# Optimization experiments

Hardware: AMD Instinct MI355X
Metric: run time of the kernel (lower is better)

## Reference

```python
import jax, jax.numpy as jnp
import numpy as np

D_MODEL = 512
N_HEADS = 8
HEAD_DIM = D_MODEL // N_HEADS
SIGMA = 0.05
LOW_RANK = 8


def setup_inputs() -> dict:
    key = jax.random.key(0)
    ks = jax.random.split(key, 16)
    B, N, Q, K = 4, 8, 256, 1024
    s = 0.02
    return {
        "query": jax.random.normal(ks[0], (B, N, Q, D_MODEL), jnp.float32),
        "key_value": jax.random.normal(ks[1], (B, N, K, D_MODEL), jnp.float32),
        "query_pos": jax.random.uniform(ks[2], (B, Q, 3), jnp.float32),
        "key_pos": jax.random.uniform(ks[3], (B, K, 3), jnp.float32),
        "key_mask": jnp.ones((B, K), dtype=bool),
        "Wq": jax.random.normal(ks[4], (D_MODEL, D_MODEL), jnp.float32) * s,
        "bq": jnp.zeros((D_MODEL,), jnp.float32),
        "Wk": jax.random.normal(ks[5], (D_MODEL, D_MODEL), jnp.float32) * s,
        "bk": jnp.zeros((D_MODEL,), jnp.float32),
        "Wv": jax.random.normal(ks[6], (D_MODEL, D_MODEL), jnp.float32) * s,
        "bv": jnp.zeros((D_MODEL,), jnp.float32),
        "Wo": jax.random.normal(ks[7], (D_MODEL, D_MODEL), jnp.float32) * s,
        "bo": jnp.zeros((D_MODEL,), jnp.float32),
        "Wqb": jax.random.normal(ks[8], (3, LOW_RANK), jnp.float32) * 0.5,
        "Wkb": jax.random.normal(ks[9], (3, LOW_RANK), jnp.float32) * 0.5,
    }


def reference(query, key_value, query_pos, key_pos, key_mask,
              Wq, bq, Wk, bk, Wv, bv, Wo, bo, Wqb, Wkb):
    B, N, Qn, _ = query.shape
    Kn = key_value.shape[2]
    scale = HEAD_DIM ** -0.5

    # projections -> [B, N, L, H, Dh]
    q = (query @ Wq + bq).reshape(B, N, Qn, N_HEADS, HEAD_DIM)
    k = (key_value @ Wk + bk).reshape(B, N, Kn, N_HEADS, HEAD_DIM)
    v = (key_value @ Wv + bv).reshape(B, N, Kn, N_HEADS, HEAD_DIM)

    logits = jnp.einsum('bnqhd,bnkhd->bnhqk', q, k) * scale

    # Gaussian distance bias: [B, Q, K]
    dist2 = jnp.sum((query_pos[:, :, None, :] - key_pos[:, None, :, :]) ** 2, axis=-1)
    sigma2 = max(SIGMA * SIGMA, 1e-6)
    dist_bias = -dist2 / (2.0 * sigma2)

    # low-rank leadfield bias: [B, Q, K]
    qb = query_pos @ Wqb  # [B, Q, R]
    kb = key_pos @ Wkb    # [B, K, R]
    lf_bias = jnp.einsum('bqr,bkr->bqk', qb, kb) / max(float(LOW_RANK) ** 0.5, 1.0)

    logits = logits + (dist_bias + lf_bias)[:, None, None, :, :]
    logits = jnp.where(key_mask[:, None, None, None, :], logits, -10000.0)

    attn = jax.nn.softmax(logits, axis=-1)
    out = jnp.einsum('bnhqk,bnkhd->bnqhd', attn, v).reshape(B, N, Qn, D_MODEL)
    return out @ Wo + bo
```

## Files before the change

kernel.cpp:

```cpp
#include <hip/hip_runtime.h>
#include <hip/hip_bf16.h>
#include <stdint.h>


typedef __attribute__((ext_vector_type(8))) short bf16x8;
typedef __attribute__((ext_vector_type(4))) float f32x4;
typedef __attribute__((ext_vector_type(2))) float f32x2;

__device__ __forceinline__ unsigned short f2b(float f){
    unsigned int u = __builtin_bit_cast(unsigned int, f);
    unsigned int r = u + 0x7fffu + ((u >> 16) & 1u);
    return (unsigned short)(r >> 16);
}
__device__ __forceinline__ float b2f(unsigned short h){
    unsigned int u = ((unsigned int)h) << 16;
    return __builtin_bit_cast(float, u);
}

__device__ __forceinline__ unsigned cvtpk2(float lo, float hi){
    unsigned r;
    asm("v_cvt_pk_bf16_f32 %0, %1, %2" : "=v"(r) : "v"(lo), "v"(hi));
    return r;
}

__device__ __forceinline__ int swz(int row, int byteInRow){
    return row*128 + (byteInRow ^ ((row & 7) << 4));
}

#define GLDS16(g, l) __builtin_amdgcn_global_load_lds( \
    (const __attribute__((address_space(1))) void*)(g), \
    (__attribute__((address_space(3))) void*)(l), 16, 0, 0)

template<int CTRL>
__device__ __forceinline__ float dpp_mov(float x){
    return __builtin_bit_cast(float,
        __builtin_amdgcn_update_dpp(0, __builtin_bit_cast(int, x), CTRL, 0xF, 0xF, true));
}
__device__ __forceinline__ float grp16_sum(float x){
    x += dpp_mov<0xB1>(x);
    x += dpp_mov<0x4E>(x);
    x += dpp_mov<0x141>(x);
    x += dpp_mov<0x140>(x);
    return x;
}

__global__ __launch_bounds__(256) void wt4_kernel(
    const float* __restrict__ Wq, const float* __restrict__ Wk,
    const float* __restrict__ Wv, const float* __restrict__ Wo,
    unsigned short* __restrict__ WtBase){
    __shared__ float tile[64][65];
    int kt = blockIdx.x, nt = blockIdx.y, wsel = blockIdx.z;
    const float* W = (wsel == 0) ? Wq : (wsel == 1) ? Wk : (wsel == 2) ? Wv : Wo;
    unsigned short* Wt = WtBase + (size_t)wsel * 262144;
    int tid = threadIdx.x;
    #pragma unroll
    for(int it=0; it<16; ++it){
        int idx = it*256 + tid;
        int r = idx >> 6, c = idx & 63;
        tile[r][c] = W[(kt*64 + r)*512 + nt*64 + c];
    }
    __syncthreads();
    #pragma unroll
    for(int it=0; it<16; ++it){
        int idx = it*256 + tid;
        int r = idx >> 6, c = idx & 63;
        Wt[(nt*64 + r)*512 + kt*64 + c] = f2b(tile[c][r]);
    }
}

__global__ __launch_bounds__(256) void posfeat2_kernel(
    const float* __restrict__ qpos, const float* __restrict__ kpos,
    const float* __restrict__ Wqb,  const float* __restrict__ Wkb,
    const int* __restrict__ mask,
    unsigned short* __restrict__ qaug,
    unsigned short* __restrict__ kaug){
    const float L2E = 1.4426950408889634f;
    const float S8  = 0.35355339059327373f;
    int id = blockIdx.x*256 + threadIdx.x;
    unsigned short o[32];
    #pragma unroll
    for(int i=0;i<32;++i) o[i] = 0;
    if(id < 1024){
        const float* p = qpos + id*3;
        float x = p[0], y = p[1], z = p[2];
        float qw[3] = {400.f*x, 400.f*y, 400.f*z};
        #pragma unroll
        for(int r=0;r<8;++r){
            float qb = x*Wqb[r] + y*Wqb[8+r] + z*Wqb[16+r];
            float c  = S8*qb;
            qw[0] += c*Wkb[r];
            qw[1] += c*Wkb[8+r];
            qw[2] += c*Wkb[16+r];
        }
        #pragma unroll
        for(int i=0;i<3;++i){
            float w = qw[i]*L2E;
            unsigned short h = f2b(w);
            unsigned short lo = f2b(w - b2f(h));
            o[i*3+0] = h; o[i*3+1] = h; o[i*3+2] = lo;
        }
        o[9] = f2b(1.0f); o[10] = f2b(1.0f);
        float cq = -200.0f*(x*x + y*y + z*z)*L2E;
        unsigned short ch = f2b(cq);
        o[11] = ch; o[12] = f2b(cq - b2f(ch));
        uint4* d = reinterpret_cast<uint4*>(qaug + (size_t)id*32);
        const uint4* s = reinterpret_cast<const uint4*>(o);
        d[0]=s[0]; d[1]=s[1]; d[2]=s[2]; d[3]=s[3];
    } else if(id < 5120){
        int k = id - 1024;
        const float* p = kpos + k*3;
        float c3[3] = {p[0], p[1], p[2]};
        float n2 = -200.0f*(c3[0]*c3[0] + c3[1]*c3[1] + c3[2]*c3[2])*L2E;
        if(!mask[k]) n2 = -50000.0f;
        #pragma unroll
        for(int i=0;i<3;++i){
            unsigned short h = f2b(c3[i]);
            unsigned short lo = f2b(c3[i] - b2f(h));
            o[i*3+0] = h; o[i*3+1] = lo; o[i*3+2] = h;
        }
        unsigned short nh = f2b(n2);
        o[9] = nh; o[10] = f2b(n2 - b2f(nh));
        o[11] = f2b(1.0f); o[12] = f2b(1.0f);
        uint4* d = reinterpret_cast<uint4*>(kaug + (size_t)k*32);
        const uint4* s = reinterpret_cast<const uint4*>(o);
        d[0]=s[0]; d[1]=s[1]; d[2]=s[2]; d[3]=s[3];
    }
}

__global__ __launch_bounds__(256) void cvt_kernel(
    const float* __restrict__ in, unsigned short* __restrict__ out, int n8){
    for(int id = blockIdx.x*256 + threadIdx.x; id < n8; id += gridDim.x*256){
        const float4* ip = reinterpret_cast<const float4*>(in) + (size_t)id*2;
        float4 a = ip[0], b = ip[1];
        uint4 w;
        w.x = cvtpk2(a.x, a.y); w.y = cvtpk2(a.z, a.w);
        w.z = cvtpk2(b.x, b.y); w.w = cvtpk2(b.z, b.w);
        reinterpret_cast<uint4*>(out)[id] = w;
    }
}

template<int EPI>
__global__ __launch_bounds__(256, 4) void gemm512g(
    const unsigned short* __restrict__ A,
    const unsigned short* __restrict__ Bt,
    const float* __restrict__ bias,
    void* __restrict__ Cv, float oscale){
    __shared__ alignas(16) char sm[32768];
    char* As = sm;
    char* Bs = sm + 16384;

    int nwg = gridDim.x;
    int q8  = nwg >> 3;
    int bid = blockIdx.x;
    int wgid = (bid & 7)*q8 + (bid >> 3);
    int n0 = (wgid & 3)*128, m0 = (wgid >> 2)*128;

    int tid = threadIdx.x;
    int l = tid & 63, wid = tid >> 6;
    int wr = wid >> 1, wc = wid & 1;
    int l15 = l & 15, lg = l >> 4;

    int srow8 = l >> 3;
    int scolb = ((l & 7) ^ srow8) << 4;

    f32x4 acc[4][4];
    const f32x4 z4 = {0.f,0.f,0.f,0.f};
    #pragma unroll
    for(int m=0;m<4;++m)
        #pragma unroll
        for(int n=0;n<4;++n) acc[m][n] = z4;

    for(int kt=0; kt<8; ++kt){
        int k0 = kt*64;
        __syncthreads();
        #pragma unroll
        for(int i=0;i<4;++i){
            int row = wid*32 + i*8 + srow8;
            const char* asrc = (const char*)(A  + (size_t)(m0+row)*512 + k0) + scolb;
            const char* bsrc = (const char*)(Bt + (size_t)(n0+row)*512 + k0) + scolb;
            GLDS16(asrc, As + wid*4096 + i*1024);
            GLDS16(bsrc, Bs + wid*4096 + i*1024);
        }
        __syncthreads();
        #pragma unroll
        for(int kk=0; kk<2; ++kk){
            bf16x8 af[4], bfr[4];
            #pragma unroll
            for(int m=0;m<4;++m)
                af[m] = *reinterpret_cast<const bf16x8*>(As + swz(wr*64 + m*16 + l15, kk*64 + lg*16));
            #pragma unroll
            for(int n=0;n<4;++n)
                bfr[n] = *reinterpret_cast<const bf16x8*>(Bs + swz(wc*64 + n*16 + l15, kk*64 + lg*16));
            #pragma unroll
            for(int m=0;m<4;++m)
                #pragma unroll
                for(int n=0;n<4;++n)
                    acc[m][n] = __builtin_amdgcn_mfma_f32_16x16x32_bf16(af[m], bfr[n], acc[m][n], 0, 0, 0);
        }
    }

    #pragma unroll
    for(int m=0;m<4;++m){
        int row = m0 + wr*64 + m*16 + lg*4;
        #pragma unroll
        for(int n=0;n<4;++n){
            int col = n0 + wc*64 + n*16 + l15;
            float bv = bias[col];
            #pragma unroll
            for(int j=0;j<4;++j){
                float val = (acc[m][n][j] + bv) * oscale;
                if(EPI == 0)
                    reinterpret_cast<unsigned short*>(Cv)[(size_t)(row+j)*512 + col] = f2b(val);
                else
                    reinterpret_cast<float*>(Cv)[(size_t)(row+j)*512 + col] = val;
            }
        }
    }
}

__global__ __launch_bounds__(256, 4) void gemm_kv2(
    const unsigned short* __restrict__ A,
    const unsigned short* __restrict__ BtKV,
    const float* __restrict__ bk_, const float* __restrict__ bv_,
    unsigned short* __restrict__ kp,
    unsigned short* __restrict__ vpT){
    __shared__ alignas(16) char sm[32768];
    char* As = sm;
    char* Bs = sm + 16384;

    int nwg = gridDim.x;
    int q8  = nwg >> 3;
    int bid = blockIdx.x;
    int wgid = (bid & 7)*q8 + (bid >> 3);
    int n0 = (wgid & 7)*128, m0 = (wgid >> 3)*128;

    int tid = threadIdx.x;
    int l = tid & 63, wid = tid >> 6;
    int wr = wid >> 1, wc = wid & 1;
    int l15 = l & 15, lg = l >> 4;

    int srow8 = l >> 3;
    int scolb = ((l & 7) ^ srow8) << 4;

    f32x4 acc[4][4];
    const f32x4 z4 = {0.f,0.f,0.f,0.f};
    #pragma unroll
    for(int m=0;m<4;++m)
        #pragma unroll
        for(int n=0;n<4;++n) acc[m][n] = z4;

    for(int kt=0; kt<8; ++kt){
        int k0 = kt*64;
        __syncthreads();
        #pragma unroll
        for(int i=0;i<4;++i){
            int row = wid*32 + i*8 + srow8;
            const char* asrc = (const char*)(A    + (size_t)(m0+row)*512 + k0) + scolb;
            const char* bsrc = (const char*)(BtKV + (size_t)(n0+row)*512 + k0) + scolb;
            GLDS16(asrc, As + wid*4096 + i*1024);
            GLDS16(bsrc, Bs + wid*4096 + i*1024);
        }
        __syncthreads();
        #pragma unroll
        for(int kk=0; kk<2; ++kk){
            bf16x8 af[4], bfr[4];
            #pragma unroll
            for(int m=0;m<4;++m)
                af[m] = *reinterpret_cast<const bf16x8*>(As + swz(wr*64 + m*16 + l15, kk*64 + lg*16));
            #pragma unroll
            for(int n=0;n<4;++n)
                bfr[n] = *reinterpret_cast<const bf16x8*>(Bs + swz(wc*64 + n*16 + l15, kk*64 + lg*16));
            #pragma unroll
            for(int m=0;m<4;++m)
                #pragma unroll
                for(int n=0;n<4;++n)
                    acc[m][n] = __builtin_amdgcn_mfma_f32_16x16x32_bf16(af[m], bfr[n], acc[m][n], 0, 0, 0);
        }
    }

    if(n0 < 512){
        #pragma unroll
        for(int m=0;m<4;++m){
            int row = m0 + wr*64 + m*16 + lg*4;
            #pragma unroll
            for(int n=0;n<4;++n){
                int col = n0 + wc*64 + n*16 + l15;
                float bv = bk_[col];
                #pragma unroll
                for(int j=0;j<4;++j)
                    kp[(size_t)(row+j)*512 + col] = f2b(acc[m][n][j] + bv);
            }
        }
    } else {
        int z = m0 >> 10;
        #pragma unroll
        for(int m=0;m<4;++m){
            int kloc = (m0 & 1023) + wr*64 + m*16 + lg*4;
            #pragma unroll
            for(int n=0;n<4;++n){
                int col = n0 - 512 + wc*64 + n*16 + l15;
                float bv = bv_[col];
                int vrow = (z*8 + (col >> 6))*64 + (col & 63);
                uint2 w;
                w.x = cvtpk2(acc[m][n][0] + bv, acc[m][n][1] + bv);
                w.y = cvtpk2(acc[m][n][2] + bv, acc[m][n][3] + bv);
                *reinterpret_cast<uint2*>(vpT + (size_t)vrow*1024 + kloc) = w;
            }
        }
    }
}

__global__ __launch_bounds__(512) void attn9_kernel(
    const unsigned short* __restrict__ qp,
    const unsigned short* __restrict__ kp,
    const unsigned short* __restrict__ vpT,
    const unsigned short* __restrict__ qaug,
    const unsigned short* __restrict__ kaug,
    unsigned short* __restrict__ ctxb){
    __shared__ alignas(16) char sm[57344];
    char* KsA = sm;
    char* KsB = sm + 8192;
    char* VsA = sm + 16384;
    char* VsB = sm + 24576;
    char* FsA = sm + 32768;
    char* FsB = sm + 36864;
    char* Ps  = sm + 40960;

    int bid = blockIdx.x;
    int xcd = bid & 7, idx = bid >> 3;
    int zh = xcd*32 + (idx >> 1), qs = idx & 1;
    int z = zh >> 3, h = zh & 7;
    int b = z >> 3;
    int tid = threadIdx.x, l = tid & 63, wid = tid >> 6;
    int l15 = l & 15, lg = l >> 4;

    const unsigned short* kbase = kp  + (size_t)(z*1024)*512 + h*64;
    const unsigned short* vbase = vpT + (size_t)((z*8+h)*64)*1024;
    char* Pw = Ps + wid*2048;
    int qbase = z*256 + qs*128 + wid*16;

    int r8 = tid >> 3;
    int csrc = ((tid & 7) ^ (r8 & 7)) << 4;
    const char* kSrc = (const char*)kbase + (size_t)r8*1024 + csrc;
    const char* vSrc = (const char*)vbase + (size_t)r8*2048 + csrc;
    int fk = (tid & 255) >> 2, fslot = tid & 3;
    const char* fSrc = (const char*)(kaug + (size_t)(b*1024 + fk)*32)
                       + ((fslot ^ ((fk >> 1) & 3)) << 4);

    bf16x8 qf[2];
    #pragma unroll
    for(int kk=0;kk<2;++kk)
        qf[kk] = *reinterpret_cast<const bf16x8*>(
            qp + (size_t)(qbase + l15)*512 + h*64 + kk*32 + lg*8);
    bf16x8 qfa = *reinterpret_cast<const bf16x8*>(
        qaug + (size_t)(b*256 + qs*128 + wid*16 + l15)*32 + lg*8);

    f32x4 psum;
    f32x4 acc[4];
    const f32x4 z4 = {0.f,0.f,0.f,0.f};
    psum = z4;
    #pragma unroll
    for(int t=0;t<4;++t) acc[t] = z4;

    auto stage = [&](int kt, char* Ks, char* Vs, char* Fs){
        GLDS16(kSrc + (size_t)kt*65536, Ks + wid*1024);
        GLDS16(vSrc + (size_t)kt*128,   Vs + wid*1024);
        if(wid < 4) GLDS16(fSrc + (size_t)kt*4096, Fs + wid*1024);
    };

    auto body = [&](int kt, const char* Ks, const char* Vs, const char* Fs){
        f32x4 s[4];
        #pragma unroll
        for(int t=0;t<4;++t){
            bf16x8 kfa = *reinterpret_cast<const bf16x8*>(
                Fs + (t*16 + l15)*64 + ((lg ^ ((l15 >> 1) & 3)) << 4));
            s[t] = __builtin_amdgcn_mfma_f32_16x16x32_bf16(qfa, kfa, z4, 0, 0, 0);
        }
        __builtin_amdgcn_s_setprio(1);
        #pragma unroll
        for(int kk=0;kk<2;++kk){
            bf16x8 kf[4];
            #pragma unroll
            for(int t=0;t<4;++t)
                kf[t] = *reinterpret_cast<const bf16x8*>(Ks + swz(t*16 + l15, kk*64 + lg*16));
            #pragma unroll
            for(int t=0;t<4;++t)
                s[t] = __builtin_amdgcn_mfma_f32_16x16x32_bf16(qf[kk], kf[t], s[t], 0, 0, 0);
        }
        __builtin_amdgcn_s_setprio(0);

        #pragma unroll
        for(int t=0;t<4;++t){
            float p0 = exp2f(s[t][0]);
            float p1 = exp2f(s[t][1]);
            float p2 = exp2f(s[t][2]);
            float p3 = exp2f(s[t][3]);
            psum += (f32x4){p0, p1, p2, p3};
            unsigned w01 = cvtpk2(p0, p1);
            unsigned w23 = cvtpk2(p2, p3);
            int cb = (t*16 + l15)*2;
            int row0 = lg*4;
            *reinterpret_cast<unsigned short*>(Pw + swz(row0+0, cb)) = (unsigned short)w01;
            *reinterpret_cast<unsigned short*>(Pw + swz(row0+1, cb)) = (unsigned short)(w01 >> 16);
            *reinterpret_cast<unsigned short*>(Pw + swz(row0+2, cb)) = (unsigned short)w23;
            *reinterpret_cast<unsigned short*>(Pw + swz(row0+3, cb)) = (unsigned short)(w23 >> 16);
        }
        #pragma unroll
        for(int kk=0;kk<2;++kk){
            bf16x8 vf[4];
            #pragma unroll
            for(int t=0;t<4;++t)
                vf[t] = *reinterpret_cast<const bf16x8*>(Vs + swz(t*16 + l15, kk*64 + lg*16));
            bf16x8 pa = *reinterpret_cast<const bf16x8*>(Pw + swz(l15, kk*64 + lg*16));
            __builtin_amdgcn_s_setprio(1);
            #pragma unroll
            for(int t=0;t<4;++t)
                acc[t] = __builtin_amdgcn_mfma_f32_16x16x32_bf16(pa, vf[t], acc[t], 0, 0, 0);
            __builtin_amdgcn_s_setprio(0);
        }
    };

    stage(0, KsA, VsA, FsA);
    #pragma unroll 1
    for(int kt=0; kt<16; kt+=2){
        __syncthreads();
        stage(kt+1, KsB, VsB, FsB);
        body(kt, KsA, VsA, FsA);
        __syncthreads();
        if(kt < 14) stage(kt+2, KsA, VsA, FsA);
        body(kt+1, KsB, VsB, FsB);
    }

    float rl[4];
    #pragma unroll
    for(int j=0;j<4;++j) rl[j] = 1.0f / grp16_sum(psum[j]);
    #pragma unroll
    for(int j=0;j<4;++j){
        int row = qbase + lg*4 + j;
        #pragma unroll
        for(int t=0;t<4;++t)
            ctxb[(size_t)row*512 + h*64 + t*16 + l15] = f2b(acc[t][j] * rl[j]);
    }
}

extern "C" void kernel_launch(void* const* d_in, const int* in_sizes, int n_in,
                              void* d_out, int out_size, void* d_ws, size_t ws_size,
                              hipStream_t stream){
    (void)in_sizes; (void)n_in; (void)out_size; (void)ws_size;
    const float* query     = (const float*)d_in[0];
    const float* key_value = (const float*)d_in[1];
    const float* query_pos = (const float*)d_in[2];
    const float* key_pos   = (const float*)d_in[3];
    const int*   key_mask  = (const int*)d_in[4];
    const float* Wq  = (const float*)d_in[5];
    const float* bq  = (const float*)d_in[6];
    const float* Wk  = (const float*)d_in[7];
    const float* bk  = (const float*)d_in[8];
    const float* Wv  = (const float*)d_in[9];
    const float* bv  = (const float*)d_in[10];
    const float* Wo  = (const float*)d_in[11];
    const float* bo  = (const float*)d_in[12];
    const float* Wqb = (const float*)d_in[13];
    const float* Wkb = (const float*)d_in[14];

    const float SCALE2 = 0.18033688011112042f;

    char* ws = (char*)d_ws;
    const size_t MB = 1048576;
    unsigned short* kp    = (unsigned short*)(ws);
    unsigned short* vpT   = (unsigned short*)(ws + 32*MB);
    unsigned short* qp    = (unsigned short*)(ws + 64*MB);
    unsigned short* kvb   = (unsigned short*)(ws + 72*MB);
    unsigned short* ctxb  = (unsigned short*)(ws + 72*MB);
    unsigned short* WtQ   = (unsigned short*)(ws + 88*MB);
    unsigned short* WtK   = WtQ + 262144;
    unsigned short* WtO   = WtQ + 3*262144;
    unsigned short* qaug  = (unsigned short*)(ws + 90*MB);
    unsigned short* kaug  = (unsigned short*)(ws + 90*MB + 65536);
    unsigned short* qb    = (unsigned short*)d_out;

    wt4_kernel<<<dim3(8,8,4), 256, 0, stream>>>(Wq, Wk, Wv, Wo, WtQ);
    posfeat2_kernel<<<20, 256, 0, stream>>>(query_pos, key_pos, Wqb, Wkb, key_mask, qaug, kaug);

    cvt_kernel<<<2048, 256, 0, stream>>>(query, qb, 524288);
    gemm512g<0><<<256, 256, 0, stream>>>(qb, WtQ, bq, qp, SCALE2);

    for(int c=0; c<2; ++c){
        const float* kvc = key_value + (size_t)c*16384*512;
        cvt_kernel<<<2048, 256, 0, stream>>>(kvc, kvb, 1048576);
        gemm_kv2<<<1024, 256, 0, stream>>>(kvb, WtK, bk, bv,
                                           kp + (size_t)c*16384*512,
                                           vpT + (size_t)c*8388608);
    }

    attn9_kernel<<<512, 512, 0, stream>>>(qp, kp, vpT, qaug, kaug, ctxb);

    gemm512g<1><<<256, 256, 0, stream>>>(ctxb, WtO, bo, d_out, 1.0f);
}
```

Measured before the change: 140.7 us.

## Halve attention block waves, each wave handles 32 query rows

```diff
diff --git a/kernel.cpp b/kernel.cpp
--- a/kernel.cpp
+++ b/kernel.cpp
@@ -310,7 +310,7 @@
     }
 }
 
-__global__ __launch_bounds__(512) void attn9_kernel(
+__global__ __launch_bounds__(256) void attn10_kernel(
     const unsigned short* __restrict__ qp,
     const unsigned short* __restrict__ kp,
     const unsigned short* __restrict__ vpT,
@@ -336,45 +336,57 @@
 
     const unsigned short* kbase = kp  + (size_t)(z*1024)*512 + h*64;
     const unsigned short* vbase = vpT + (size_t)((z*8+h)*64)*1024;
-    char* Pw = Ps + wid*2048;
-    int qbase = z*256 + qs*128 + wid*16;
+    char* Pw = Ps + wid*4096;
+    int qbase = z*256 + qs*128 + wid*32;
 
     int r8 = tid >> 3;
     int csrc = ((tid & 7) ^ (r8 & 7)) << 4;
-    const char* kSrc = (const char*)kbase + (size_t)r8*1024 + csrc;
-    const char* vSrc = (const char*)vbase + (size_t)r8*2048 + csrc;
-    int fk = (tid & 255) >> 2, fslot = tid & 3;
+    const char* kSrc  = (const char*)kbase + (size_t)r8*1024 + csrc;
+    const char* kSrc2 = kSrc + 32*1024;
+    const char* vSrc  = (const char*)vbase + (size_t)r8*2048 + csrc;
+    const char* vSrc2 = vSrc + 32*2048;
+    int fk = tid >> 2, fslot = tid & 3;
     const char* fSrc = (const char*)(kaug + (size_t)(b*1024 + fk)*32)
                        + ((fslot ^ ((fk >> 1) & 3)) << 4);
 
-    bf16x8 qf[2];
-    #pragma unroll
-    for(int kk=0;kk<2;++kk)
-        qf[kk] = *reinterpret_cast<const bf16x8*>(
-            qp + (size_t)(qbase + l15)*512 + h*64 + kk*32 + lg*8);
-    bf16x8 qfa = *reinterpret_cast<const bf16x8*>(
-        qaug + (size_t)(b*256 + qs*128 + wid*16 + l15)*32 + lg*8);
-
-    f32x4 psum;
-    f32x4 acc[4];
+    bf16x8 qf[2][2];
+    bf16x8 qfa[2];
+    #pragma unroll
+    for(int qh=0;qh<2;++qh){
+        #pragma unroll
+        for(int kk=0;kk<2;++kk)
+            qf[qh][kk] = *reinterpret_cast<const bf16x8*>(
+                qp + (size_t)(qbase + qh*16 + l15)*512 + h*64 + kk*32 + lg*8);
+        qfa[qh] = *reinterpret_cast<const bf16x8*>(
+            qaug + (size_t)(b*256 + qs*128 + wid*32 + qh*16 + l15)*32 + lg*8);
+    }
+
+    f32x4 psum[2];
+    f32x4 acc[2][4];
     const f32x4 z4 = {0.f,0.f,0.f,0.f};
-    psum = z4;
-    #pragma unroll
-    for(int t=0;t<4;++t) acc[t] = z4;
+    #pragma unroll
+    for(int qh=0;qh<2;++qh){
+        psum[qh] = z4;
+        #pragma unroll
+        for(int t=0;t<4;++t) acc[qh][t] = z4;
+    }
 
     auto stage = [&](int kt, char* Ks, char* Vs, char* Fs){
-        GLDS16(kSrc + (size_t)kt*65536, Ks + wid*1024);
-        GLDS16(vSrc + (size_t)kt*128,   Vs + wid*1024);
-        if(wid < 4) GLDS16(fSrc + (size_t)kt*4096, Fs + wid*1024);
+        GLDS16(kSrc  + (size_t)kt*65536, Ks + wid*1024);
+        GLDS16(kSrc2 + (size_t)kt*65536, Ks + 4096 + wid*1024);
+        GLDS16(vSrc  + (size_t)kt*128,   Vs + wid*1024);
+        GLDS16(vSrc2 + (size_t)kt*128,   Vs + 4096 + wid*1024);
+        GLDS16(fSrc  + (size_t)kt*4096,  Fs + wid*1024);
     };
 
     auto body = [&](int kt, const char* Ks, const char* Vs, const char* Fs){
-        f32x4 s[4];
+        f32x4 s[2][4];
         #pragma unroll
         for(int t=0;t<4;++t){
             bf16x8 kfa = *reinterpret_cast<const bf16x8*>(
                 Fs + (t*16 + l15)*64 + ((lg ^ ((l15 >> 1) & 3)) << 4));
-            s[t] = __builtin_amdgcn_mfma_f32_16x16x32_bf16(qfa, kfa, z4, 0, 0, 0);
+            s[0][t] = __builtin_amdgcn_mfma_f32_16x16x32_bf16(qfa[0], kfa, z4, 0, 0, 0);
+            s[1][t] = __builtin_amdgcn_mfma_f32_16x16x32_bf16(qfa[1], kfa, z4, 0, 0, 0);
         }
         __builtin_amdgcn_s_setprio(1);
         #pragma unroll
@@ -384,26 +396,31 @@
             for(int t=0;t<4;++t)
                 kf[t] = *reinterpret_cast<const bf16x8*>(Ks + swz(t*16 + l15, kk*64 + lg*16));
             #pragma unroll
-            for(int t=0;t<4;++t)
-                s[t] = __builtin_amdgcn_mfma_f32_16x16x32_bf16(qf[kk], kf[t], s[t], 0, 0, 0);
+            for(int t=0;t<4;++t){
+                s[0][t] = __builtin_amdgcn_mfma_f32_16x16x32_bf16(qf[0][kk], kf[t], s[0][t], 0, 0, 0);
+                s[1][t] = __builtin_amdgcn_mfma_f32_16x16x32_bf16(qf[1][kk], kf[t], s[1][t], 0, 0, 0);
+            }
         }
         __builtin_amdgcn_s_setprio(0);
 
         #pragma unroll
-        for(int t=0;t<4;++t){
-            float p0 = exp2f(s[t][0]);
-            float p1 = exp2f(s[t][1]);
-            float p2 = exp2f(s[t][2]);
-            float p3 = exp2f(s[t][3]);
-            psum += (f32x4){p0, p1, p2, p3};
-            unsigned w01 = cvtpk2(p0, p1);
-            unsigned w23 = cvtpk2(p2, p3);
-            int cb = (t*16 + l15)*2;
-            int row0 = lg*4;
-            *reinterpret_cast<unsigned short*>(Pw + swz(row0+0, cb)) = (unsigned short)w01;
-            *reinterpret_cast<unsigned short*>(Pw + swz(row0+1, cb)) = (unsigned short)(w01 >> 16);
-            *reinterpret_cast<unsigned short*>(Pw + swz(row0+2, cb)) = (unsigned short)w23;
-            *reinterpret_cast<unsigned short*>(Pw + swz(row0+3, cb)) = (unsigned short)(w23 >> 16);
+        for(int qh=0;qh<2;++qh){
+            int row0 = qh*16 + lg*4;
+            #pragma unroll
+            for(int t=0;t<4;++t){
+                float p0 = exp2f(s[qh][t][0]);
+                float p1 = exp2f(s[qh][t][1]);
+                float p2 = exp2f(s[qh][t][2]);
+                float p3 = exp2f(s[qh][t][3]);
+                psum[qh] += (f32x4){p0, p1, p2, p3};
+                unsigned w01 = cvtpk2(p0, p1);
+                unsigned w23 = cvtpk2(p2, p3);
+                int cb = (t*16 + l15)*2;
+                *reinterpret_cast<unsigned short*>(Pw + swz(row0+0, cb)) = (unsigned short)w01;
+                *reinterpret_cast<unsigned short*>(Pw + swz(row0+1, cb)) = (unsigned short)(w01 >> 16);
+                *reinterpret_cast<unsigned short*>(Pw + swz(row0+2, cb)) = (unsigned short)w23;
+                *reinterpret_cast<unsigned short*>(Pw + swz(row0+3, cb)) = (unsigned short)(w23 >> 16);
+            }
         }
         #pragma unroll
         for(int kk=0;kk<2;++kk){
@@ -411,11 +428,14 @@
             #pragma unroll
             for(int t=0;t<4;++t)
                 vf[t] = *reinterpret_cast<const bf16x8*>(Vs + swz(t*16 + l15, kk*64 + lg*16));
-            bf16x8 pa = *reinterpret_cast<const bf16x8*>(Pw + swz(l15, kk*64 + lg*16));
             __builtin_amdgcn_s_setprio(1);
             #pragma unroll
-            for(int t=0;t<4;++t)
-                acc[t] = __builtin_amdgcn_mfma_f32_16x16x32_bf16(pa, vf[t], acc[t], 0, 0, 0);
+            for(int qh=0;qh<2;++qh){
+                bf16x8 pa = *reinterpret_cast<const bf16x8*>(Pw + swz(qh*16 + l15, kk*64 + lg*16));
+                #pragma unroll
+                for(int t=0;t<4;++t)
+                    acc[qh][t] = __builtin_amdgcn_mfma_f32_16x16x32_bf16(pa, vf[t], acc[qh][t], 0, 0, 0);
+            }
             __builtin_amdgcn_s_setprio(0);
         }
     };
@@ -431,15 +451,18 @@
         body(kt+1, KsB, VsB, FsB);
     }
 
-    float rl[4];
-    #pragma unroll
-    for(int j=0;j<4;++j) rl[j] = 1.0f / grp16_sum(psum[j]);
-    #pragma unroll
-    for(int j=0;j<4;++j){
-        int row = qbase + lg*4 + j;
-        #pragma unroll
-        for(int t=0;t<4;++t)
-            ctxb[(size_t)row*512 + h*64 + t*16 + l15] = f2b(acc[t][j] * rl[j]);
+    #pragma unroll
+    for(int qh=0;qh<2;++qh){
+        float rl[4];
+        #pragma unroll
+        for(int j=0;j<4;++j) rl[j] = 1.0f / grp16_sum(psum[qh][j]);
+        #pragma unroll
+        for(int j=0;j<4;++j){
+            int row = qbase + qh*16 + lg*4 + j;
+            #pragma unroll
+            for(int t=0;t<4;++t)
+                ctxb[(size_t)row*512 + h*64 + t*16 + l15] = f2b(acc[qh][t][j] * rl[j]);
+        }
     }
 }
 
@@ -493,7 +516,7 @@
                                            vpT + (size_t)c*8388608);
     }
 
-    attn9_kernel<<<512, 512, 0, stream>>>(qp, kp, vpT, qaug, kaug, ctxb);
+    attn10_kernel<<<512, 256, 0, stream>>>(qp, kp, vpT, qaug, kaug, ctxb);
 
     gemm512g<1><<<256, 256, 0, stream>>>(ctxb, WtO, bo, d_out, 1.0f);
 }
```

New measurement: 143.2 us. Within noise of the previous version (+1.8%).

## Fuse fp32-to-bf16 conversion into projection GEMM tile loads

Applied to the files above, without the earlier changes.

```diff
diff --git a/kernel.cpp b/kernel.cpp
--- a/kernel.cpp
+++ b/kernel.cpp
@@ -5,7 +5,6 @@
 
 typedef __attribute__((ext_vector_type(8))) short bf16x8;
 typedef __attribute__((ext_vector_type(4))) float f32x4;
-typedef __attribute__((ext_vector_type(2))) float f32x2;
 
 __device__ __forceinline__ unsigned short f2b(float f){
     unsigned int u = __builtin_bit_cast(unsigned int, f);
@@ -127,18 +126,6 @@
     }
 }
 
-__global__ __launch_bounds__(256) void cvt_kernel(
-    const float* __restrict__ in, unsigned short* __restrict__ out, int n8){
-    for(int id = blockIdx.x*256 + threadIdx.x; id < n8; id += gridDim.x*256){
-        const float4* ip = reinterpret_cast<const float4*>(in) + (size_t)id*2;
-        float4 a = ip[0], b = ip[1];
-        uint4 w;
-        w.x = cvtpk2(a.x, a.y); w.y = cvtpk2(a.z, a.w);
-        w.z = cvtpk2(b.x, b.y); w.w = cvtpk2(b.z, b.w);
-        reinterpret_cast<uint4*>(out)[id] = w;
-    }
-}
-
 template<int EPI>
 __global__ __launch_bounds__(256, 4) void gemm512g(
     const unsigned short* __restrict__ A,
@@ -218,8 +205,90 @@
     }
 }
 
-__global__ __launch_bounds__(256, 4) void gemm_kv2(
-    const unsigned short* __restrict__ A,
+__global__ __launch_bounds__(256, 3) void gemm512f(
+    const float* __restrict__ A,
+    const unsigned short* __restrict__ Bt,
+    const float* __restrict__ bias,
+    unsigned short* __restrict__ C, float oscale){
+    __shared__ alignas(16) char sm[32768];
+    char* As = sm;
+    char* Bs = sm + 16384;
+
+    int nwg = gridDim.x;
+    int q8  = nwg >> 3;
+    int bid = blockIdx.x;
+    int wgid = (bid & 7)*q8 + (bid >> 3);
+    int n0 = (wgid & 3)*128, m0 = (wgid >> 2)*128;
+
+    int tid = threadIdx.x;
+    int l = tid & 63, wid = tid >> 6;
+    int wr = wid >> 1, wc = wid & 1;
+    int l15 = l & 15, lg = l >> 4;
+
+    int srow8 = l >> 3;
+    int scolb = ((l & 7) ^ srow8) << 4;
+
+    f32x4 acc[4][4];
+    const f32x4 z4 = {0.f,0.f,0.f,0.f};
+    #pragma unroll
+    for(int m=0;m<4;++m)
+        #pragma unroll
+        for(int n=0;n<4;++n) acc[m][n] = z4;
+
+    for(int kt=0; kt<8; ++kt){
+        int k0 = kt*64;
+        __syncthreads();
+        #pragma unroll
+        for(int it=0; it<8; ++it){
+            int idx = it*256 + tid;
+            int row = idx >> 4;
+            int col = (idx & 15) * 4;
+            float4 v = *reinterpret_cast<const float4*>(A + (size_t)(m0+row)*512 + k0 + col);
+            uint2 d;
+            d.x = cvtpk2(v.x, v.y);
+            d.y = cvtpk2(v.z, v.w);
+            *reinterpret_cast<uint2*>(As + swz(row, col*2)) = d;
+        }
+        #pragma unroll
+        for(int i=0;i<4;++i){
+            int row = wid*32 + i*8 + srow8;
+            const char* bsrc = (const char*)(Bt + (size_t)(n0+row)*512 + k0) + scolb;
+            GLDS16(bsrc, Bs + wid*4096 + i*1024);
+        }
+        __syncthreads();
+        #pragma unroll
+        for(int kk=0; kk<2; ++kk){
+            bf16x8 af[4], bfr[4];
+            #pragma unroll
+            for(int m=0;m<4;++m)
+                af[m] = *reinterpret_cast<const bf16x8*>(As + swz(wr*64 + m*16 + l15, kk*64 + lg*16));
+            #pragma unroll
+            for(int n=0;n<4;++n)
+                bfr[n] = *reinterpret_cast<const bf16x8*>(Bs + swz(wc*64 + n*16 + l15, kk*64 + lg*16));
+            #pragma unroll
+            for(int m=0;m<4;++m)
+                #pragma unroll
+                for(int n=0;n<4;++n)
+                    acc[m][n] = __builtin_amdgcn_mfma_f32_16x16x32_bf16(af[m], bfr[n], acc[m][n], 0, 0, 0);
+        }
+    }
+
+    #pragma unroll
+    for(int m=0;m<4;++m){
+        int row = m0 + wr*64 + m*16 + lg*4;
+        #pragma unroll
+        for(int n=0;n<4;++n){
+            int col = n0 + wc*64 + n*16 + l15;
+            float bv = bias[col];
+            #pragma unroll
+            for(int j=0;j<4;++j)
+                C[(size_t)(row+j)*512 + col] = f2b((acc[m][n][j] + bv) * oscale);
+        }
+    }
+}
+
+__global__ __launch_bounds__(256, 3) void gemm_kvF(
+    const float* __restrict__ A,
     const unsigned short* __restrict__ BtKV,
     const float* __restrict__ bk_, const float* __restrict__ bv_,
     unsigned short* __restrict__ kp,
@@ -253,11 +322,20 @@
         int k0 = kt*64;
         __syncthreads();
         #pragma unroll
+        for(int it=0; it<8; ++it){
+            int idx = it*256 + tid;
+            int row = idx >> 4;
+            int col = (idx & 15) * 4;
+            float4 v = *reinterpret_cast<const float4*>(A + (size_t)(m0+row)*512 + k0 + col);
+            uint2 d;
+            d.x = cvtpk2(v.x, v.y);
+            d.y = cvtpk2(v.z, v.w);
+            *reinterpret_cast<uint2*>(As + swz(row, col*2)) = d;
+        }
+        #pragma unroll
         for(int i=0;i<4;++i){
             int row = wid*32 + i*8 + srow8;
-            const char* asrc = (const char*)(A    + (size_t)(m0+row)*512 + k0) + scolb;
             const char* bsrc = (const char*)(BtKV + (size_t)(n0+row)*512 + k0) + scolb;
-            GLDS16(asrc, As + wid*4096 + i*1024);
             GLDS16(bsrc, Bs + wid*4096 + i*1024);
         }
         __syncthreads();
@@ -470,28 +548,19 @@
     unsigned short* kp    = (unsigned short*)(ws);
     unsigned short* vpT   = (unsigned short*)(ws + 32*MB);
     unsigned short* qp    = (unsigned short*)(ws + 64*MB);
-    unsigned short* kvb   = (unsigned short*)(ws + 72*MB);
     unsigned short* ctxb  = (unsigned short*)(ws + 72*MB);
-    unsigned short* WtQ   = (unsigned short*)(ws + 88*MB);
+    unsigned short* WtQ   = (unsigned short*)(ws + 80*MB);
     unsigned short* WtK   = WtQ + 262144;
     unsigned short* WtO   = WtQ + 3*262144;
-    unsigned short* qaug  = (unsigned short*)(ws + 90*MB);
-    unsigned short* kaug  = (unsigned short*)(ws + 90*MB + 65536);
-    unsigned short* qb    = (unsigned short*)d_out;
+    unsigned short* qaug  = (unsigned short*)(ws + 82*MB);
+    unsigned short* kaug  = (unsigned short*)(ws + 82*MB + 65536);
 
     wt4_kernel<<<dim3(8,8,4), 256, 0, stream>>>(Wq, Wk, Wv, Wo, WtQ);
     posfeat2_kernel<<<20, 256, 0, stream>>>(query_pos, key_pos, Wqb, Wkb, key_mask, qaug, kaug);
 
-    cvt_kernel<<<2048, 256, 0, stream>>>(query, qb, 524288);
-    gemm512g<0><<<256, 256, 0, stream>>>(qb, WtQ, bq, qp, SCALE2);
-
-    for(int c=0; c<2; ++c){
-        const float* kvc = key_value + (size_t)c*16384*512;
-        cvt_kernel<<<2048, 256, 0, stream>>>(kvc, kvb, 1048576);
-        gemm_kv2<<<1024, 256, 0, stream>>>(kvb, WtK, bk, bv,
-                                           kp + (size_t)c*16384*512,
-                                           vpT + (size_t)c*8388608);
-    }
+    gemm512f<<<256, 256, 0, stream>>>(query, WtQ, bq, qp, SCALE2);
+
+    gemm_kvF<<<2048, 256, 0, stream>>>(key_value, WtK, bk, bv, kp, vpT);
 
     attn9_kernel<<<512, 512, 0, stream>>>(qp, kp, vpT, qaug, kaug, ctxb);
 
```

Result: slower. 158.1 us (+12.4%).
